# Performance work log

Measured on AMD Instinct MI355X. Metric: run time of the kernel, lower is better.

Reference implementation:

```python
import jax, jax.numpy as jnp
import numpy as np

WS = 8            # window size (square)
HEADS = 16
HEAD_DIM = 32
DIM = 512
NEG_INF = float('-inf')


def _create_mask(ws, disp, upper_lower, left_right):
    size = ws * ws
    m = np.zeros((size, size), dtype=np.float32)
    d = disp
    if upper_lower:
        m[-d * ws:, :-d * ws] = NEG_INF
        m[:-d * ws, -d * ws:] = NEG_INF
    if left_right:
        m = m.reshape(ws, ws, ws, ws)
        m[:, -d:, :, :-d] = NEG_INF
        m[:, :-d, :, -d:] = NEG_INF
        m = m.reshape(size, size)
    return m


def _relative_indices(ws):
    coords = np.array([[x, y] for x in range(ws) for y in range(ws)])  # [ws^2, 2]
    dist = coords[None, :, :] - coords[:, None, :]                      # [ws^2, ws^2, 2]
    dist += ws - 1
    return dist.astype(np.int64)


_REL_IDX = _relative_indices(WS)                      # [64, 64, 2]
_UL_MASK = jnp.asarray(_create_mask(WS, WS // 2, True, False))   # [64, 64]
_LR_MASK = jnp.asarray(_create_mask(WS, WS // 2, False, True))   # [64, 64]


def setup_inputs() -> dict:
    key = jax.random.key(0)
    ks = jax.random.split(key, 5)
    b, n = 16, 64
    return {
        'x': jax.random.normal(ks[0], (b, n, n, DIM), dtype=jnp.float32),
        'w_qkv': jax.random.normal(ks[1], (3 * HEADS * HEAD_DIM, DIM), dtype=jnp.float32) * 0.02,
        'pos_embedding': jax.random.normal(ks[2], (2 * WS - 1, 2 * WS - 1), dtype=jnp.float32),
        'w_out': jax.random.normal(ks[3], (DIM, HEADS * HEAD_DIM), dtype=jnp.float32) * 0.02,
        'b_out': jax.random.normal(ks[4], (DIM,), dtype=jnp.float32) * 0.02,
    }


def reference(x, w_qkv, pos_embedding, w_out, b_out):
    disp = WS // 2
    scale = HEAD_DIM ** -0.5
    b, n_h, n_w, _ = x.shape
    nw_h, nw_w = n_h // WS, n_w // WS

    # cyclic shift (shifted=True)
    x = jnp.roll(x, shift=(-disp, -disp), axis=(1, 2))

    qkv = x @ w_qkv.T                                   # [b, n_h, n_w, 3*h*d]
    qkv = qkv.reshape(b, nw_h, WS, nw_w, WS, 3, HEADS, HEAD_DIM)
    # -> [3, b, heads, n_windows, window_tokens, head_dim]
    qkv = qkv.transpose(5, 0, 6, 1, 3, 2, 4, 7).reshape(
        3, b, HEADS, nw_h * nw_w, WS * WS, HEAD_DIM)
    q, k, v = qkv[0], qkv[1], qkv[2]

    dots = jnp.einsum('bhwid,bhwjd->bhwij', q, k) * scale
    # relative position bias
    dots = dots + pos_embedding[_REL_IDX[:, :, 0], _REL_IDX[:, :, 1]]
    # shift masks: last window-row and last window-column
    dots = dots.at[:, :, -nw_w:].add(_UL_MASK)
    dots = dots.at[:, :, nw_w - 1::nw_w].add(_LR_MASK)

    attn = jax.nn.softmax(dots, axis=-1)
    out = jnp.einsum('bhwij,bhwjd->bhwid', attn, v)     # [b,h,nw,ws^2,d]

    out = out.reshape(b, HEADS, nw_h, nw_w, WS, WS, HEAD_DIM)
    out = out.transpose(0, 2, 4, 3, 5, 1, 6).reshape(b, n_h, n_w, HEADS * HEAD_DIM)
    out = out @ w_out.T + b_out

    out = jnp.roll(out, shift=(disp, disp), axis=(1, 2))
    return out
```

## Files before the change

kernel.cpp:

```cpp
#include <hip/hip_runtime.h>
#include <hip/hip_bf16.h>
#include <stdint.h>

typedef __bf16 bf16;
typedef __attribute__((ext_vector_type(4))) float f32x4;
typedef __attribute__((ext_vector_type(8))) bf16 bf16x8;
typedef __attribute__((ext_vector_type(4))) bf16 bf16x4;

#define AS1 __attribute__((address_space(1)))
#define AS3 __attribute__((address_space(3)))

static __device__ __forceinline__ void gload_lds16(const bf16* g, bf16* l) {
  __builtin_amdgcn_global_load_lds((const AS1 void*)g, (AS3 void*)l, 16, 0, 0);
}

#define BAR __builtin_amdgcn_s_barrier()
#define LGKM0 asm volatile("s_waitcnt lgkmcnt(0)" ::: "memory")
#define VMC(n) asm volatile("s_waitcnt vmcnt(" #n ")" ::: "memory")
#define SCHED0 __builtin_amdgcn_sched_barrier(0)

#define STAGE_A(gsrc, dst, kt_) do {                                          \
  _Pragma("unroll") for (int s_ = 0; s_ < 4; ++s_) {                          \
    int idx_ = s_ * 256 + tid;                                                \
    int r_ = idx_ >> 3, c_ = idx_ & 7;                                        \
    gload_lds16((gsrc) + (size_t)r_ * 512 + ((kt_) << 6) + ((c_ ^ (r_ & 7)) << 3), \
                (dst) + idx_ * 8);                                            \
  }                                                                           \
} while (0)

#define LOADB(ktq, NCOLX) do {                                                \
  const bf16* bp_ = Bptr + (size_t)(ktq) * ((size_t)(NCOLX) * 64);            \
  _Pragma("unroll") for (int cb_ = 0; cb_ < 4; ++cb_)                         \
  _Pragma("unroll") for (int ks_ = 0; ks_ < 2; ++ks_)                         \
    bfr[cb_][ks_] = *(const bf16x8*)(bp_ + cb_ * 128 + (size_t)ks_ * (NCOLX) * 32); \
} while (0)

#define KLOOP_BD(Ag, NCOLX)                                                   \
  f32x4 acc[4][4] = {};                                                       \
  bf16x8 af[4][2], bfr[4][2];                                                 \
  STAGE_A(Ag, SA0, 0);                                                        \
  LOADB(0, NCOLX);                                                            \
  VMC(8); BAR;                 \
  STAGE_A(Ag, SA1, 1);                                                        \
  _Pragma("unroll 2")                                                         \
  for (int kt = 0; kt < 8; ++kt) {                                            \
    bf16* Ap = (kt & 1) ? SA1 : SA0;                                          \
    _Pragma("unroll") for (int i_ = 0; i_ < 4; ++i_) {                        \
      int ra_ = wr + i_ * 16 + lr;                                            \
      _Pragma("unroll") for (int ks_ = 0; ks_ < 2; ++ks_)                     \
        af[i_][ks_] = *(const bf16x8*)(Ap + ra_ * 64 + (((ks_ * 4 + lg) ^ (ra_ & 7)) << 3)); \
    }                                                                         \
    LGKM0; SCHED0;              \
    __builtin_amdgcn_s_setprio(1);                                            \
    _Pragma("unroll") for (int i_ = 0; i_ < 4; ++i_)                          \
    _Pragma("unroll") for (int j_ = 0; j_ < 4; ++j_)                          \
    _Pragma("unroll") for (int ks_ = 0; ks_ < 2; ++ks_)                       \
      acc[i_][j_] = __builtin_amdgcn_mfma_f32_16x16x32_bf16(                  \
          af[i_][ks_], bfr[j_][ks_], acc[i_][j_], 0, 0, 0);                   \
    __builtin_amdgcn_s_setprio(0);                                            \
    if (kt < 7) LOADB(kt + 1, NCOLX);    \
    if (kt < 7) { VMC(8); }           \
    BAR;                       \
    if (kt < 6) STAGE_A(Ag, Ap, kt + 2);   \
  }

__global__ __launch_bounds__(256) void prep_x(const float* __restrict__ x,
                                              bf16* __restrict__ xs) {
  int m = blockIdx.x * 8 + (threadIdx.x >> 5);
  int lane = threadIdx.x & 31;
  int b = m >> 12, win = (m >> 6) & 63, t = m & 63;
  int ip = ((win >> 3) << 3) + (t >> 3);
  int jp = ((win & 7) << 3) + (t & 7);
  int io = (ip + 4) & 63, jo = (jp + 4) & 63;
  const float* src = x + ((((size_t)(b << 6) + io) << 6) + jo) * 512;
  bf16* dst = xs + ((size_t)m << 9);
  #pragma unroll
  for (int c0 = 0; c0 < 512; c0 += 128) {
    int c = c0 + lane * 4;
    float4 v = *(const float4*)(src + c);
    bf16x4 o = { (bf16)v.x, (bf16)v.y, (bf16)v.z, (bf16)v.w };
    *(bf16x4*)(dst + c) = o;
  }
}

__global__ __launch_bounds__(256) void prep_w(const float* __restrict__ wqkv,
                                              const float* __restrict__ wout,
                                              bf16* __restrict__ wqkv_bt,
                                              bf16* __restrict__ wout_bt) {
  int r = blockIdx.x * 8 + (threadIdx.x >> 5);
  int lane = threadIdx.x & 31;
  const float* src;
  bf16* dstb;
  int ncol, col;
  float sc = 1.0f;
  if (r < 1536) {
    src = wqkv + (size_t)r * 512; dstb = wqkv_bt; ncol = 1536; col = r;
    if (r < 512) sc = 0.17677669529663689f;
  } else {
    src = wout + (size_t)(r - 1536) * 512; dstb = wout_bt; ncol = 512; col = r - 1536;
  }
  #pragma unroll
  for (int kb = lane; kb < 64; kb += 32) {
    float4 v0 = *(const float4*)(src + kb * 8);
    float4 v1 = *(const float4*)(src + kb * 8 + 4);
    bf16x8 o = { (bf16)(v0.x * sc), (bf16)(v0.y * sc), (bf16)(v0.z * sc), (bf16)(v0.w * sc),
                 (bf16)(v1.x * sc), (bf16)(v1.y * sc), (bf16)(v1.z * sc), (bf16)(v1.w * sc) };
    *(bf16x8*)(dstb + ((size_t)kb * ncol + col) * 8) = o;
  }
}

__global__ __launch_bounds__(256) void prep_bias(const float* __restrict__ pos,
                                                 float* __restrict__ bias4) {
  for (int idx = threadIdx.x; idx < 4 * 4096; idx += 256) {
    int ty = idx >> 12, ij = idx & 4095;
    int i = ij >> 6, j = ij & 63;
    int rx = ((j >> 3) - (i >> 3)) + 7;
    int ry = ((j & 7) - (i & 7)) + 7;
    float v = pos[rx * 15 + ry];
    if ((ty & 1) && (((i ^ j) >> 5) & 1)) v = -1e30f;
    if ((ty & 2) && (((i ^ j) >> 2) & 1)) v = -1e30f;
    bias4[idx] = v;
  }
}

__global__ __launch_bounds__(256, 3) void gemm_qkv(
    const bf16* __restrict__ xs, const bf16* __restrict__ wb,
    bf16* __restrict__ qb, bf16* __restrict__ kb, bf16* __restrict__ vb) {
  __shared__ union { bf16 A[2][8192]; bf16 C[128][128]; } sm;
  bf16* SA0 = sm.A[0]; bf16* SA1 = sm.A[1];

  const int tid = threadIdx.x, wave = tid >> 6, lane = tid & 63;
  int bid = blockIdx.x;
  bid = (bid & 7) * 768 + (bid >> 3);
  const int mt = bid / 12, nt = bid % 12;

  const bf16* Ag = xs + ((size_t)mt * 128) * 512;
  const int wr = (wave >> 1) << 6, wc = (wave & 1) << 6;
  const int lr = lane & 15, lg = lane >> 4;
  const bf16* Bptr = wb + (((size_t)lg * 1536) + nt * 128 + wc + lr) * 8;

  KLOOP_BD(Ag, 1536)

  #pragma unroll
  for (int i = 0; i < 4; ++i)
    #pragma unroll
    for (int j = 0; j < 4; ++j)
      #pragma unroll
      for (int r = 0; r < 4; ++r) {
        int row = wr + i * 16 + (lg << 2) + r;
        int col = wc + j * 16 + lr;
        sm.C[row][col ^ ((row & 7) << 3)] = (bf16)acc[i][j][r];
      }
  __syncthreads();
  const int sel = nt >> 2;
  #pragma unroll
  for (int ch = 0; ch < 2; ++ch) {
    int c = wave * 2 + ch;
    int wl = c >> 2, hl = c & 3;
    int gw = mt * 2 + wl;
    int b = gw >> 6, win = gw & 63;
    int h = ((nt & 3) << 2) + hl;
    size_t ubase = ((size_t)((b << 4) + h) * 64 + win) * 2048;
    if (sel < 2) {
      bf16* dst = (sel == 0 ? qb : kb) + ubase;
      #pragma unroll
      for (int p = 0; p < 4; ++p) {
        int off = p * 512 + lane * 8;
        int t = off >> 5, d = off & 31;
        int row = (wl << 6) + t, col = (hl << 5) + d;
        bf16x8 v = *(const bf16x8*)&sm.C[row][col ^ ((row & 7) << 3)];
        *(bf16x8*)(dst + off) = v;
      }
    } else {
      bf16* dst = vb + ubase;
      #pragma unroll
      for (int p = 0; p < 4; ++p) {
        int off = p * 512 + lane * 8;
        int d = off >> 6, t0 = off & 63;
        int col = (hl << 5) + d;
        bf16x8 v;
        #pragma unroll
        for (int q = 0; q < 8; ++q) {
          int row = (wl << 6) + t0 + q;
          v[q] = sm.C[row][col ^ ((row & 7) << 3)];
        }
        *(bf16x8*)(dst + off) = v;
      }
    }
  }
}

__global__ __launch_bounds__(256) void attn(
    const bf16* __restrict__ qb, const bf16* __restrict__ kb,
    const bf16* __restrict__ vb, const float* __restrict__ bias4,
    bf16* __restrict__ ao) {
  __shared__ bf16 Ps[4][64][72];
  const int wave = threadIdx.x >> 6, lane = threadIdx.x & 63;
  const int u = blockIdx.x * 4 + wave;
  const int b = u >> 10, h = (u >> 6) & 15, win = u & 63;
  const int lr = lane & 15, lg = lane >> 4;

  const bf16* qu = qb + (size_t)u * 2048;
  const bf16* ku = kb + (size_t)u * 2048;
  const bf16* vu = vb + (size_t)u * 2048;

  bf16x8 qf[4], kf[4];
  #pragma unroll
  for (int i = 0; i < 4; ++i) {
    qf[i] = *(const bf16x8*)(qu + (i * 16 + lr) * 32 + (lg << 3));
    kf[i] = *(const bf16x8*)(ku + (i * 16 + lr) * 32 + (lg << 3));
  }
  f32x4 s[4][4] = {};
  #pragma unroll
  for (int i = 0; i < 4; ++i)
    #pragma unroll
    for (int j = 0; j < 4; ++j)
      s[i][j] = __builtin_amdgcn_mfma_f32_16x16x32_bf16(qf[i], kf[j], s[i][j], 0, 0, 0);

  const int ty = ((win >= 56) ? 1 : 0) | (((win & 7) == 7) ? 2 : 0);
  const float* bt = bias4 + ty * 4096;
  #pragma unroll
  for (int i = 0; i < 4; ++i)
    #pragma unroll
    for (int r = 0; r < 4; ++r) {
      int row = i * 16 + (lg << 2) + r;
      #pragma unroll
      for (int j = 0; j < 4; ++j)
        s[i][j][r] += bt[row * 64 + j * 16 + lr];
    }
  #pragma unroll
  for (int i = 0; i < 4; ++i)
    #pragma unroll
    for (int r = 0; r < 4; ++r) {
      float mx = fmaxf(fmaxf(s[i][0][r], s[i][1][r]), fmaxf(s[i][2][r], s[i][3][r]));
      mx = fmaxf(mx, __shfl_xor(mx, 1));
      mx = fmaxf(mx, __shfl_xor(mx, 2));
      mx = fmaxf(mx, __shfl_xor(mx, 4));
      mx = fmaxf(mx, __shfl_xor(mx, 8));
      float sum = 0.f;
      #pragma unroll
      for (int j = 0; j < 4; ++j) { s[i][j][r] = __expf(s[i][j][r] - mx); sum += s[i][j][r]; }
      sum += __shfl_xor(sum, 1);
      sum += __shfl_xor(sum, 2);
      sum += __shfl_xor(sum, 4);
      sum += __shfl_xor(sum, 8);
      float inv = 1.0f / sum;
      int row = i * 16 + (lg << 2) + r;
      #pragma unroll
      for (int j = 0; j < 4; ++j)
        Ps[wave][row][j * 16 + lr] = (bf16)(s[i][j][r] * inv);
    }
  f32x4 o[4][2] = {};
  #pragma unroll
  for (int kk = 0; kk < 2; ++kk) {
    bf16x8 vf[2];
    #pragma unroll
    for (int nj = 0; nj < 2; ++nj)
      vf[nj] = *(const bf16x8*)(vu + (nj * 16 + lr) * 64 + kk * 32 + (lg << 3));
    #pragma unroll
    for (int mi = 0; mi < 4; ++mi) {
      bf16x8 pa = *(const bf16x8*)&Ps[wave][mi * 16 + lr][kk * 32 + (lg << 3)];
      #pragma unroll
      for (int nj = 0; nj < 2; ++nj)
        o[mi][nj] = __builtin_amdgcn_mfma_f32_16x16x32_bf16(pa, vf[nj], o[mi][nj], 0, 0, 0);
    }
  }
  bf16* dst = ao + ((size_t)(b * 64 + win) * 64) * 512 + h * 32;
  #pragma unroll
  for (int mi = 0; mi < 4; ++mi)
    #pragma unroll
    for (int r = 0; r < 4; ++r) {
      int t = mi * 16 + (lg << 2) + r;
      #pragma unroll
      for (int nj = 0; nj < 2; ++nj)
        dst[(size_t)t * 512 + nj * 16 + lr] = (bf16)o[mi][nj][r];
    }
}

__global__ __launch_bounds__(256, 3) void gemm_out(
    const bf16* __restrict__ ao, const bf16* __restrict__ wob,
    const float* __restrict__ bout, float* __restrict__ out) {
  __shared__ bf16 SA[2][8192];
  bf16* SA0 = SA[0]; bf16* SA1 = SA[1];

  const int tid = threadIdx.x, wave = tid >> 6, lane = tid & 63;
  int bid = blockIdx.x;
  bid = (bid & 7) * 256 + (bid >> 3);
  const int mt = bid >> 2, nt = bid & 3;
  const bf16* Ag = ao + ((size_t)mt * 128) * 512;
  const int wr = (wave >> 1) << 6, wc = (wave & 1) << 6;
  const int lr = lane & 15, lg = lane >> 4;
  const bf16* Bptr = wob + (((size_t)lg * 512) + nt * 128 + wc + lr) * 8;

  KLOOP_BD(Ag, 512)

  float bv[4];
  #pragma unroll
  for (int j = 0; j < 4; ++j) bv[j] = bout[nt * 128 + wc + j * 16 + lr];
  #pragma unroll
  for (int i = 0; i < 4; ++i)
    #pragma unroll
    for (int r = 0; r < 4; ++r) {
      int m = (mt << 7) + wr + i * 16 + (lg << 2) + r;
      int b = m >> 12, win = (m >> 6) & 63, t = m & 63;
      int ip = ((win >> 3) << 3) + (t >> 3);
      int jp = ((win & 7) << 3) + (t & 7);
      int io = (ip + 4) & 63, jo = (jp + 4) & 63;
      float* orow = out + ((((size_t)(b << 6) + io) << 6) + jo) * 512 + nt * 128 + wc;
      #pragma unroll
      for (int j = 0; j < 4; ++j)
        orow[j * 16 + lr] = acc[i][j][r] + bv[j];
    }
}

extern "C" void kernel_launch(void* const* d_in, const int* in_sizes, int n_in,
                              void* d_out, int out_size, void* d_ws, size_t ws_size,
                              hipStream_t stream) {
  const float* x    = (const float*)d_in[0];
  const float* wqkv = (const float*)d_in[1];
  const float* pos  = (const float*)d_in[2];
  const float* wout = (const float*)d_in[3];
  const float* bout = (const float*)d_in[4];
  float* out = (float*)d_out;

  char* ws = (char*)d_ws;
  bf16* xs      = (bf16*)(ws);
  bf16* qb      = (bf16*)(ws + 67108864);
  bf16* kb      = (bf16*)(ws + 134217728);
  bf16* vb      = (bf16*)(ws + 201326592);
  bf16* wqkv_bf = (bf16*)(ws + 268435456);
  bf16* wout_bf = (bf16*)(ws + 270008320);
  float* bias4  = (float*)(ws + 270532608);

  prep_x<<<dim3(8192), dim3(256), 0, stream>>>(x, xs);
  prep_w<<<dim3(256), dim3(256), 0, stream>>>(wqkv, wout, wqkv_bf, wout_bf);
  prep_bias<<<dim3(1), dim3(256), 0, stream>>>(pos, bias4);
  gemm_qkv<<<dim3(6144), dim3(256), 0, stream>>>(xs, wqkv_bf, qb, kb, vb);
  attn<<<dim3(4096), dim3(256), 0, stream>>>(qb, kb, vb, bias4, xs);
  gemm_out<<<dim3(2048), dim3(256), 0, stream>>>(xs, wout_bf, bout, out);
}
```

Before: 307.8 us.

## Fuse QKV projection GEMM with windowed attention per head group

Merges the QKV GEMM and the attention kernel into one 512-thread kernel. Each wave computes Q, K and V for one head and one 64-token window, then runs attention directly from LDS, so the Q/K/V intermediates never go to global memory. The QKV weight columns are reordered per head (q, k, v interleaved) so one block's N-tile covers whole heads. The cost is larger register use per wave (a 4x6 accumulator tile) and occupancy limited to one 512-thread block per CU.

```diff
diff --git a/kernel.cpp b/kernel.cpp
--- a/kernel.cpp
+++ b/kernel.cpp
@@ -28,6 +28,15 @@
   }                                                                           \
 } while (0)
 
+#define STAGE_A2(gsrc, dst, kt_) do {                                         \
+  _Pragma("unroll") for (int s_ = 0; s_ < 2; ++s_) {                          \
+    int idx_ = s_ * 512 + tid;                                                \
+    int r_ = idx_ >> 3, c_ = idx_ & 7;                                        \
+    gload_lds16((gsrc) + (size_t)r_ * 512 + ((kt_) << 6) + ((c_ ^ (r_ & 7)) << 3), \
+                (dst) + idx_ * 8);                                            \
+  }                                                                           \
+} while (0)
+
 #define LOADB(ktq, NCOLX) do {                                                \
   const bf16* bp_ = Bptr + (size_t)(ktq) * ((size_t)(NCOLX) * 64);            \
   _Pragma("unroll") for (int cb_ = 0; cb_ < 4; ++cb_)                         \
@@ -35,12 +44,19 @@
     bfr[cb_][ks_] = *(const bf16x8*)(bp_ + cb_ * 128 + (size_t)ks_ * (NCOLX) * 32); \
 } while (0)
 
+#define LOADB6(ktq) do {                                                      \
+  const bf16* bp_ = Bptr + (size_t)(ktq) * 98304;                             \
+  _Pragma("unroll") for (int cb_ = 0; cb_ < 6; ++cb_)                         \
+  _Pragma("unroll") for (int ks_ = 0; ks_ < 2; ++ks_)                         \
+    bfr[cb_][ks_] = *(const bf16x8*)(bp_ + cb_ * 128 + ks_ * 49152);          \
+} while (0)
+
 #define KLOOP_BD(Ag, NCOLX)                                                   \
   f32x4 acc[4][4] = {};                                                       \
   bf16x8 af[4][2], bfr[4][2];                                                 \
   STAGE_A(Ag, SA0, 0);                                                        \
   LOADB(0, NCOLX);                                                            \
-  VMC(8); BAR;                 \
+  VMC(8); BAR;                                                                \
   STAGE_A(Ag, SA1, 1);                                                        \
   _Pragma("unroll 2")                                                         \
   for (int kt = 0; kt < 8; ++kt) {                                            \
@@ -50,7 +66,7 @@
       _Pragma("unroll") for (int ks_ = 0; ks_ < 2; ++ks_)                     \
         af[i_][ks_] = *(const bf16x8*)(Ap + ra_ * 64 + (((ks_ * 4 + lg) ^ (ra_ & 7)) << 3)); \
     }                                                                         \
-    LGKM0; SCHED0;              \
+    LGKM0; SCHED0;                                                            \
     __builtin_amdgcn_s_setprio(1);                                            \
     _Pragma("unroll") for (int i_ = 0; i_ < 4; ++i_)                          \
     _Pragma("unroll") for (int j_ = 0; j_ < 4; ++j_)                          \
@@ -58,10 +74,10 @@
       acc[i_][j_] = __builtin_amdgcn_mfma_f32_16x16x32_bf16(                  \
           af[i_][ks_], bfr[j_][ks_], acc[i_][j_], 0, 0, 0);                   \
     __builtin_amdgcn_s_setprio(0);                                            \
-    if (kt < 7) LOADB(kt + 1, NCOLX);    \
-    if (kt < 7) { VMC(8); }           \
-    BAR;                       \
-    if (kt < 6) STAGE_A(Ag, Ap, kt + 2);   \
+    if (kt < 7) LOADB(kt + 1, NCOLX);                                         \
+    if (kt < 7) { VMC(8); }                                                   \
+    BAR;                                                                      \
+    if (kt < 6) STAGE_A(Ag, Ap, kt + 2);                                      \
   }
 
 __global__ __launch_bounds__(256) void prep_x(const float* __restrict__ x,
@@ -94,8 +110,10 @@
   int ncol, col;
   float sc = 1.0f;
   if (r < 1536) {
-    src = wqkv + (size_t)r * 512; dstb = wqkv_bt; ncol = 1536; col = r;
-    if (r < 512) sc = 0.17677669529663689f;
+    int part = r >> 9, h = (r >> 5) & 15, d = r & 31;
+    src = wqkv + (size_t)r * 512; dstb = wqkv_bt; ncol = 1536;
+    col = h * 96 + part * 32 + d;
+    if (part == 0) sc = 0.17677669529663689f;
   } else {
     src = wout + (size_t)(r - 1536) * 512; dstb = wout_bt; ncol = 512; col = r - 1536;
   }
@@ -123,92 +141,80 @@
   }
 }
 
-__global__ __launch_bounds__(256, 3) void gemm_qkv(
-    const bf16* __restrict__ xs, const bf16* __restrict__ wb,
-    bf16* __restrict__ qb, bf16* __restrict__ kb, bf16* __restrict__ vb) {
-  __shared__ union { bf16 A[2][8192]; bf16 C[128][128]; } sm;
+__global__ __launch_bounds__(512, 1) void qkv_attn(
+    const bf16* __restrict__ xs, const bf16* __restrict__ wb2,
+    const float* __restrict__ bias4, bf16* __restrict__ ao) {
+  __shared__ union { bf16 A[2][8192]; bf16 E[8][6144]; } sm;
   bf16* SA0 = sm.A[0]; bf16* SA1 = sm.A[1];
 
   const int tid = threadIdx.x, wave = tid >> 6, lane = tid & 63;
+  const int ww = wave & 1, wh = wave >> 1;
+  const int lr = lane & 15, lg = lane >> 4;
+
   int bid = blockIdx.x;
-  bid = (bid & 7) * 768 + (bid >> 3);
-  const int mt = bid / 12, nt = bid % 12;
+  bid = (bid & 7) * 256 + (bid >> 3);
+  const int mt = bid >> 2, hg = bid & 3;
+  const int h = hg * 4 + wh;
 
   const bf16* Ag = xs + ((size_t)mt * 128) * 512;
-  const int wr = (wave >> 1) << 6, wc = (wave & 1) << 6;
-  const int lr = lane & 15, lg = lane >> 4;
-  const bf16* Bptr = wb + (((size_t)lg * 1536) + nt * 128 + wc + lr) * 8;
-
-  KLOOP_BD(Ag, 1536)
-
-  #pragma unroll
-  for (int i = 0; i < 4; ++i)
-    #pragma unroll
-    for (int j = 0; j < 4; ++j)
-      #pragma unroll
-      for (int r = 0; r < 4; ++r) {
-        int row = wr + i * 16 + (lg << 2) + r;
-        int col = wc + j * 16 + lr;
-        sm.C[row][col ^ ((row & 7) << 3)] = (bf16)acc[i][j][r];
+  const bf16* Bptr = wb2 + (((size_t)lg * 1536) + h * 96 + lr) * 8;
+
+  f32x4 acc[4][6] = {};
+  bf16x8 af[4][2], bfr[6][2];
+
+  STAGE_A2(Ag, SA0, 0);
+  LOADB6(0);
+  VMC(12); BAR;
+  STAGE_A2(Ag, SA1, 1);
+  #pragma unroll 2
+  for (int kt = 0; kt < 8; ++kt) {
+    bf16* Ap = (kt & 1) ? SA1 : SA0;
+    #pragma unroll
+    for (int i_ = 0; i_ < 4; ++i_) {
+      int ra_ = ww * 64 + i_ * 16 + lr;
+      #pragma unroll
+      for (int ks_ = 0; ks_ < 2; ++ks_)
+        af[i_][ks_] = *(const bf16x8*)(Ap + ra_ * 64 + (((ks_ * 4 + lg) ^ (ra_ & 7)) << 3));
+    }
+    LGKM0; SCHED0;
+    __builtin_amdgcn_s_setprio(1);
+    #pragma unroll
+    for (int i_ = 0; i_ < 4; ++i_)
+      #pragma unroll
+      for (int j_ = 0; j_ < 6; ++j_)
+        #pragma unroll
+        for (int ks_ = 0; ks_ < 2; ++ks_)
+          acc[i_][j_] = __builtin_amdgcn_mfma_f32_16x16x32_bf16(
+              af[i_][ks_], bfr[j_][ks_], acc[i_][j_], 0, 0, 0);
+    __builtin_amdgcn_s_setprio(0);
+    if (kt < 7) { LOADB6(kt + 1); VMC(12); }
+    BAR;
+    if (kt < 6) STAGE_A2(Ag, Ap, kt + 2);
+  }
+  bf16* Ew = sm.E[wave];
+  #pragma unroll
+  for (int i = 0; i < 4; ++i)
+    #pragma unroll
+    for (int r = 0; r < 4; ++r) {
+      int row = i * 16 + (lg << 2) + r;
+      #pragma unroll
+      for (int j = 0; j < 4; ++j) {
+        int c = j * 16 + lr;
+        Ew[row * 64 + (c ^ ((row & 7) << 3))] = (bf16)acc[i][j][r];
       }
-  __syncthreads();
-  const int sel = nt >> 2;
-  #pragma unroll
-  for (int ch = 0; ch < 2; ++ch) {
-    int c = wave * 2 + ch;
-    int wl = c >> 2, hl = c & 3;
-    int gw = mt * 2 + wl;
-    int b = gw >> 6, win = gw & 63;
-    int h = ((nt & 3) << 2) + hl;
-    size_t ubase = ((size_t)((b << 4) + h) * 64 + win) * 2048;
-    if (sel < 2) {
-      bf16* dst = (sel == 0 ? qb : kb) + ubase;
-      #pragma unroll
-      for (int p = 0; p < 4; ++p) {
-        int off = p * 512 + lane * 8;
-        int t = off >> 5, d = off & 31;
-        int row = (wl << 6) + t, col = (hl << 5) + d;
-        bf16x8 v = *(const bf16x8*)&sm.C[row][col ^ ((row & 7) << 3)];
-        *(bf16x8*)(dst + off) = v;
+      #pragma unroll
+      for (int j = 4; j < 6; ++j) {
+        int cv = (j - 4) * 16 + lr;
+        Ew[4096 + cv * 64 + (row ^ ((cv & 7) << 3))] = (bf16)acc[i][j][r];
       }
-    } else {
-      bf16* dst = vb + ubase;
-      #pragma unroll
-      for (int p = 0; p < 4; ++p) {
-        int off = p * 512 + lane * 8;
-        int d = off >> 6, t0 = off & 63;
-        int col = (hl << 5) + d;
-        bf16x8 v;
-        #pragma unroll
-        for (int q = 0; q < 8; ++q) {
-          int row = (wl << 6) + t0 + q;
-          v[q] = sm.C[row][col ^ ((row & 7) << 3)];
-        }
-        *(bf16x8*)(dst + off) = v;
-      }
-    }
-  }
-}
-
-__global__ __launch_bounds__(256) void attn(
-    const bf16* __restrict__ qb, const bf16* __restrict__ kb,
-    const bf16* __restrict__ vb, const float* __restrict__ bias4,
-    bf16* __restrict__ ao) {
-  __shared__ bf16 Ps[4][64][72];
-  const int wave = threadIdx.x >> 6, lane = threadIdx.x & 63;
-  const int u = blockIdx.x * 4 + wave;
-  const int b = u >> 10, h = (u >> 6) & 15, win = u & 63;
-  const int lr = lane & 15, lg = lane >> 4;
-
-  const bf16* qu = qb + (size_t)u * 2048;
-  const bf16* ku = kb + (size_t)u * 2048;
-  const bf16* vu = vb + (size_t)u * 2048;
-
+    }
+  LGKM0; SCHED0;
   bf16x8 qf[4], kf[4];
   #pragma unroll
   for (int i = 0; i < 4; ++i) {
-    qf[i] = *(const bf16x8*)(qu + (i * 16 + lr) * 32 + (lg << 3));
-    kf[i] = *(const bf16x8*)(ku + (i * 16 + lr) * 32 + (lg << 3));
+    int ra = i * 16 + lr;
+    qf[i] = *(const bf16x8*)(Ew + ra * 64 + (((lg << 3)) ^ ((ra & 7) << 3)));
+    kf[i] = *(const bf16x8*)(Ew + ra * 64 + ((32 + (lg << 3)) ^ ((ra & 7) << 3)));
   }
   f32x4 s[4][4] = {};
   #pragma unroll
@@ -217,6 +223,8 @@
     for (int j = 0; j < 4; ++j)
       s[i][j] = __builtin_amdgcn_mfma_f32_16x16x32_bf16(qf[i], kf[j], s[i][j], 0, 0, 0);
 
+  const int gw = mt * 2 + ww;
+  const int win = gw & 63;
   const int ty = ((win >= 56) ? 1 : 0) | (((win & 7) == 7) ? 2 : 0);
   const float* bt = bias4 + ty * 4096;
   #pragma unroll
@@ -247,25 +255,31 @@
       float inv = 1.0f / sum;
       int row = i * 16 + (lg << 2) + r;
       #pragma unroll
-      for (int j = 0; j < 4; ++j)
-        Ps[wave][row][j * 16 + lr] = (bf16)(s[i][j][r] * inv);
-    }
+      for (int j = 0; j < 4; ++j) {
+        int c = j * 16 + lr;
+        Ew[row * 64 + (c ^ ((row & 7) << 3))] = (bf16)(s[i][j][r] * inv);
+      }
+    }
+  LGKM0; SCHED0;
   f32x4 o[4][2] = {};
   #pragma unroll
   for (int kk = 0; kk < 2; ++kk) {
     bf16x8 vf[2];
     #pragma unroll
-    for (int nj = 0; nj < 2; ++nj)
-      vf[nj] = *(const bf16x8*)(vu + (nj * 16 + lr) * 64 + kk * 32 + (lg << 3));
+    for (int nj = 0; nj < 2; ++nj) {
+      int dv = nj * 16 + lr;
+      vf[nj] = *(const bf16x8*)(Ew + 4096 + dv * 64 + ((kk * 32 + (lg << 3)) ^ ((dv & 7) << 3)));
+    }
     #pragma unroll
     for (int mi = 0; mi < 4; ++mi) {
-      bf16x8 pa = *(const bf16x8*)&Ps[wave][mi * 16 + lr][kk * 32 + (lg << 3)];
+      int ra = mi * 16 + lr;
+      bf16x8 pa = *(const bf16x8*)(Ew + ra * 64 + ((kk * 32 + (lg << 3)) ^ ((ra & 7) << 3)));
       #pragma unroll
       for (int nj = 0; nj < 2; ++nj)
         o[mi][nj] = __builtin_amdgcn_mfma_f32_16x16x32_bf16(pa, vf[nj], o[mi][nj], 0, 0, 0);
     }
   }
-  bf16* dst = ao + ((size_t)(b * 64 + win) * 64) * 512 + h * 32;
+  bf16* dst = ao + ((size_t)(mt * 128 + ww * 64)) * 512 + h * 32;
   #pragma unroll
   for (int mi = 0; mi < 4; ++mi)
     #pragma unroll
@@ -325,17 +339,14 @@
 
   char* ws = (char*)d_ws;
   bf16* xs      = (bf16*)(ws);
-  bf16* qb      = (bf16*)(ws + 67108864);
-  bf16* kb      = (bf16*)(ws + 134217728);
-  bf16* vb      = (bf16*)(ws + 201326592);
-  bf16* wqkv_bf = (bf16*)(ws + 268435456);
-  bf16* wout_bf = (bf16*)(ws + 270008320);
+  bf16* ao      = (bf16*)(ws + 67108864);
+  bf16* wqkv_bt = (bf16*)(ws + 268435456);
+  bf16* wout_bt = (bf16*)(ws + 270008320);
   float* bias4  = (float*)(ws + 270532608);
 
   prep_x<<<dim3(8192), dim3(256), 0, stream>>>(x, xs);
-  prep_w<<<dim3(256), dim3(256), 0, stream>>>(wqkv, wout, wqkv_bf, wout_bf);
+  prep_w<<<dim3(256), dim3(256), 0, stream>>>(wqkv, wout, wqkv_bt, wout_bt);
   prep_bias<<<dim3(1), dim3(256), 0, stream>>>(pos, bias4);
-  gemm_qkv<<<dim3(6144), dim3(256), 0, stream>>>(xs, wqkv_bf, qb, kb, vb);
-  attn<<<dim3(4096), dim3(256), 0, stream>>>(qb, kb, vb, bias4, xs);
-  gemm_out<<<dim3(2048), dim3(256), 0, stream>>>(xs, wout_bf, bout, out);
-}
+  qkv_attn<<<dim3(2048), dim3(512), 0, stream>>>(xs, wqkv_bt, bias4, ao);
+  gemm_out<<<dim3(2048), dim3(256), 0, stream>>>(ao, wout_bt, bout, out);
+}
```

After: 266.3 us. 1.16x faster.
